# Performance work log

Measured on AMD Instinct MI355X. Metric: run time of the kernel, lower is better.

Reference implementation:

```python
import jax, jax.numpy as jnp
import numpy as np

LAMBDA_WEIGHT = 1.0


def _soft_argmax(logits):
    # differentiable_argmax: sum_c softmax(logits)[c] * c along class dim
    nc = logits.shape[1]
    probs = jax.nn.softmax(logits, axis=1)
    idx = jnp.arange(nc, dtype=logits.dtype)[None, :, None, None]
    return jnp.sum(probs * idx, axis=1)  # [B, H, W]


def _pair_loss(mask, d):
    # mask: [L] bool over row-major flattened HxW; d: [L] float (col - row).
    # torch.where returns row-major order, coord[:,1]-coord[:,0] == d at masked
    # pixels; second diff is |d_i - d_prev| over consecutive masked pixels.
    L = mask.shape[0]
    pos = jnp.where(mask, jnp.arange(L), -1)
    last = jax.lax.cummax(pos, axis=0)                 # last masked index <= i
    prev = jnp.concatenate([jnp.full((1,), -1), last[:-1]])  # strictly before i
    valid = mask & (prev >= 0)
    dprev = d[jnp.clip(prev, 0, L - 1)]
    s = jnp.sum(jnp.where(valid, jnp.abs(d - dprev), 0.0))
    npairs = jnp.sum(valid)
    npts = jnp.sum(mask)
    mean = s / jnp.maximum(npairs, 1).astype(d.dtype)
    # N==0 contributes 0 (the `continue`); N==1 gives an empty-mean (NaN) in
    # torch -- guarded to 0 here (such degenerate classes are skipped).
    return jnp.where(npts >= 2, mean / (npts + 1).astype(d.dtype), 0.0)


def reference(logits, labels):
    bs, nc, h, w = logits.shape
    seg = jnp.floor(jax.lax.stop_gradient(_soft_argmax(logits))).astype(jnp.int32)
    seg = seg.reshape(bs, h * w)                       # [B, L] row-major
    # d[i] = col - row for flattened index i
    i = jnp.arange(h * w)
    d = ((i % w) - (i // w)).astype(jnp.float32)       # [L]
    classes = jnp.arange(1, nc, dtype=jnp.int32)       # skip background c=0
    masks = seg[:, None, :] == classes[None, :, None]  # [B, nc-1, L]
    per = jax.vmap(jax.vmap(_pair_loss, in_axes=(0, None)), in_axes=(0, None))(masks, d)
    return jnp.sum(per) * LAMBDA_WEIGHT


def setup_inputs() -> dict:
    key = jax.random.key(0)
    k1, k2 = jax.random.split(key)
    logits = jax.random.normal(k1, (16, 7, 368, 640), dtype=jnp.float32)
    labels = jax.random.randint(k2, (16, 368, 640), 0, 7, dtype=jnp.int64)
    return {"logits": logits, "labels": labels}
```

## Files before the change

### kernel.cpp

```cpp
#include <hip/hip_runtime.h>
#include <cstdint>
#include <cstddef>

#define BB 16
#define CC 7
#define HH 368
#define WW 640
#define LL (HH * WW)
#define NCLS 6
#define NCOMBO (BB * NCLS)
#define PXW 256
#define PXB 1024
#define BPB (LL / PXB)
#define NBLK (BB * BPB)

struct St { int S, cnt, first, last; };

__device__ inline St comb(const St& a, const St& b) {
    St r;
    int both = (a.cnt > 0) & (b.cnt > 0);
    r.S     = a.S + b.S + (both ? abs(b.first - a.last) : 0);
    r.cnt   = a.cnt + b.cnt;
    r.first = (a.cnt > 0) ? a.first : b.first;
    r.last  = (b.cnt > 0) ? b.last : a.last;
    return r;
}

__device__ inline St shfl_down_st(const St& s, int off) {
    St r;
    r.S     = __shfl_down(s.S, off, 64);
    r.cnt   = __shfl_down(s.cnt, off, 64);
    r.first = __shfl_down(s.first, off, 64);
    r.last  = __shfl_down(s.last, off, 64);
    return r;
}

__global__ __launch_bounds__(256) void fused_kernel(const float* __restrict__ logits,
                                                    int4* __restrict__ blkStates) {
    int blk = blockIdx.x;
    int b   = blk / BPB;
    int bb  = blk - b * BPB;
    int t   = threadIdx.x;
    int w   = t >> 6;
    int lane = t & 63;
    int i   = bb * PXB + w * PXW + lane * 4;
    const float* base = logits + (size_t)b * CC * LL + i;

    float x[CC][4];
#pragma unroll
    for (int c = 0; c < CC; ++c) {
        float4 v = *reinterpret_cast<const float4*>(base + (size_t)c * LL);
        x[c][0] = v.x; x[c][1] = v.y; x[c][2] = v.z; x[c][3] = v.w;
    }

    int row = i / WW;
    int col = i - row * WW;
    int d0  = col - row;

    St st[NCLS];
#pragma unroll
    for (int c = 0; c < NCLS; ++c) { st[c].S = 0; st[c].cnt = 0; st[c].first = 0; st[c].last = 0; }

#pragma unroll
    for (int k = 0; k < 4; ++k) {
        float m = x[0][k];
#pragma unroll
        for (int c = 1; c < CC; ++c) m = fmaxf(m, x[c][k]);
        float s = 0.0f, wsum = 0.0f;
#pragma unroll
        for (int c = 0; c < CC; ++c) {
            float e = __expf(x[c][k] - m);
            s += e;
            wsum += e * (float)c;
        }
        int sv = (int)floorf(__fdividef(wsum, s));
        int d  = d0 + k;
#pragma unroll
        for (int c = 0; c < NCLS; ++c) {
            if (sv == c + 1) {
                if (st[c].cnt == 0) st[c].first = d;
                else                st[c].S += abs(d - st[c].last);
                st[c].last = d;
                st[c].cnt++;
            }
        }
    }

    __shared__ int4 sw[NCLS][4];

#pragma unroll
    for (int c = 0; c < NCLS; ++c) {
        St s = st[c];
        if (__ballot(s.cnt > 0) == 0ull) {
            if (lane == 0) sw[c][w] = make_int4(0, 0, 0, 0);
            continue;
        }
#pragma unroll
        for (int off = 1; off < 64; off <<= 1) {
            St o = shfl_down_st(s, off);
            s = comb(s, o);
        }
        if (lane == 0) sw[c][w] = make_int4(s.S, s.cnt, s.first, s.last);
    }
    __syncthreads();

    if (t < NCLS) {
        St acc{sw[t][0].x, sw[t][0].y, sw[t][0].z, sw[t][0].w};
#pragma unroll
        for (int q = 1; q < 4; ++q) {
            St o{sw[t][q].x, sw[t][q].y, sw[t][q].z, sw[t][q].w};
            acc = comb(acc, o);
        }
        blkStates[(size_t)t * NBLK + blk] = make_int4(acc.S, acc.cnt, acc.first, acc.last);
    }
}

__global__ __launch_bounds__(256) void combine_kernel(const int4* __restrict__ blkStates,
                                                      float* __restrict__ out) {
    int combo = blockIdx.x;
    int b = combo / NCLS;
    int c = combo - b * NCLS;
    int t = threadIdx.x;

    St st{0, 0, 0, 0};
    if (t < BPB) {
        int4 v = blkStates[(size_t)c * NBLK + b * BPB + t];
        st = St{v.x, v.y, v.z, v.w};
    }

#pragma unroll
    for (int off = 1; off < 64; off <<= 1) {
        St o = shfl_down_st(st, off);
        st = comb(st, o);
    }

    __shared__ int4 ws[4];
    int wave = t >> 6;
    if ((t & 63) == 0) ws[wave] = make_int4(st.S, st.cnt, st.first, st.last);
    __syncthreads();

    if (t == 0) {
        St acc{ws[0].x, ws[0].y, ws[0].z, ws[0].w};
#pragma unroll
        for (int w = 1; w < 4; ++w) {
            St o{ws[w].x, ws[w].y, ws[w].z, ws[w].w};
            acc = comb(acc, o);
        }
        int n = acc.cnt;
        if (n >= 2) {
            double res = ((double)acc.S / (double)(n - 1)) / (double)(n + 1);
            atomicAdd(out, (float)res);
        }
    }
}

extern "C" void kernel_launch(void* const* d_in, const int* in_sizes, int n_in,
                              void* d_out, int out_size, void* d_ws, size_t ws_size,
                              hipStream_t stream) {
    const float* logits = (const float*)d_in[0];
    float* out = (float*)d_out;

    int4* blkStates = (int4*)d_ws;

    hipMemsetAsync(out, 0, sizeof(float) * out_size, stream);
    fused_kernel<<<NBLK, 256, 0, stream>>>(logits, blkStates);
    combine_kernel<<<NCOMBO, 256, 0, stream>>>(blkStates, out);
}
```

Before: 166.7 us.

## Process larger tiles per block with shared-memory seg staging and sequential per-thread scan

Each block now handles 5120 pixels: it first computes soft-argmax labels coalesced into packed bytes in shared memory, then each thread scans 20 consecutive pixels serially before the wave and block reductions. This cuts the block count and the number of per-class shuffle reductions per pixel, and it lets the combine kernel use a single wave with no shared-memory stage. In exchange it adds a shared-memory round trip and a barrier. The per-thread serial loop over 20 pixels and 6 classes may also raise register use and branch divergence.

```diff
diff --git a/kernel.cpp b/kernel.cpp
--- a/kernel.cpp
+++ b/kernel.cpp
@@ -9,10 +9,10 @@
 #define LL (HH * WW)
 #define NCLS 6
 #define NCOMBO (BB * NCLS)
-#define PXW 256
-#define PXB 1024
-#define BPB (LL / PXB)
+#define TILE 5120
+#define BPB (LL / TILE)
 #define NBLK (BB * BPB)
+#define PPT (TILE / 256)
 
 struct St { int S, cnt, first, last; };
 
@@ -43,37 +43,58 @@
     int t   = threadIdx.x;
     int w   = t >> 6;
     int lane = t & 63;
-    int i   = bb * PXB + w * PXW + lane * 4;
-    const float* base = logits + (size_t)b * CC * LL + i;
 
-    float x[CC][4];
+    __shared__ uint32_t segw[TILE / 4];
+    __shared__ int4 sw[NCLS][4];
+
+    const float* lbase = logits + (size_t)b * CC * LL;
+
 #pragma unroll
-    for (int c = 0; c < CC; ++c) {
-        float4 v = *reinterpret_cast<const float4*>(base + (size_t)c * LL);
-        x[c][0] = v.x; x[c][1] = v.y; x[c][2] = v.z; x[c][3] = v.w;
+    for (int j = 0; j < TILE / 1024; ++j) {
+        int px = bb * TILE + j * 1024 + t * 4;
+        const float* base = lbase + px;
+        float x[CC][4];
+#pragma unroll
+        for (int c = 0; c < CC; ++c) {
+            float4 v = *reinterpret_cast<const float4*>(base + (size_t)c * LL);
+            x[c][0] = v.x; x[c][1] = v.y; x[c][2] = v.z; x[c][3] = v.w;
+        }
+        uint32_t packed = 0;
+#pragma unroll
+        for (int k = 0; k < 4; ++k) {
+            float m = x[0][k];
+#pragma unroll
+            for (int c = 1; c < CC; ++c) m = fmaxf(m, x[c][k]);
+            float s = 0.0f, wsum = 0.0f;
+#pragma unroll
+            for (int c = 0; c < CC; ++c) {
+                float e = __expf(x[c][k] - m);
+                s += e;
+                wsum += e * (float)c;
+            }
+            int sv = (int)floorf(__fdividef(wsum, s));
+            packed |= (uint32_t)sv << (8 * k);
+        }
+        segw[j * 256 + t] = packed;
     }
+    __syncthreads();
 
-    int row = i / WW;
-    int col = i - row * WW;
+    int gpx = bb * TILE + t * PPT;
+    int row = gpx / WW;
+    int col = gpx - row * WW;
     int d0  = col - row;
+
+    uint32_t wbuf[PPT / 4];
+#pragma unroll
+    for (int j = 0; j < PPT / 4; ++j) wbuf[j] = segw[t * (PPT / 4) + j];
 
     St st[NCLS];
 #pragma unroll
     for (int c = 0; c < NCLS; ++c) { st[c].S = 0; st[c].cnt = 0; st[c].first = 0; st[c].last = 0; }
 
 #pragma unroll
-    for (int k = 0; k < 4; ++k) {
-        float m = x[0][k];
-#pragma unroll
-        for (int c = 1; c < CC; ++c) m = fmaxf(m, x[c][k]);
-        float s = 0.0f, wsum = 0.0f;
-#pragma unroll
-        for (int c = 0; c < CC; ++c) {
-            float e = __expf(x[c][k] - m);
-            s += e;
-            wsum += e * (float)c;
-        }
-        int sv = (int)floorf(__fdividef(wsum, s));
+    for (int k = 0; k < PPT; ++k) {
+        int sv = (int)((wbuf[k >> 2] >> (8 * (k & 3))) & 0xFFu);
         int d  = d0 + k;
 #pragma unroll
         for (int c = 0; c < NCLS; ++c) {
@@ -86,15 +107,9 @@
         }
     }
 
-    __shared__ int4 sw[NCLS][4];
-
 #pragma unroll
     for (int c = 0; c < NCLS; ++c) {
         St s = st[c];
-        if (__ballot(s.cnt > 0) == 0ull) {
-            if (lane == 0) sw[c][w] = make_int4(0, 0, 0, 0);
-            continue;
-        }
 #pragma unroll
         for (int off = 1; off < 64; off <<= 1) {
             St o = shfl_down_st(s, off);
@@ -115,8 +130,8 @@
     }
 }
 
-__global__ __launch_bounds__(256) void combine_kernel(const int4* __restrict__ blkStates,
-                                                      float* __restrict__ out) {
+__global__ __launch_bounds__(64) void combine_kernel(const int4* __restrict__ blkStates,
+                                                     float* __restrict__ out) {
     int combo = blockIdx.x;
     int b = combo / NCLS;
     int c = combo - b * NCLS;
@@ -134,21 +149,10 @@
         st = comb(st, o);
     }
 
-    __shared__ int4 ws[4];
-    int wave = t >> 6;
-    if ((t & 63) == 0) ws[wave] = make_int4(st.S, st.cnt, st.first, st.last);
-    __syncthreads();
-
     if (t == 0) {
-        St acc{ws[0].x, ws[0].y, ws[0].z, ws[0].w};
-#pragma unroll
-        for (int w = 1; w < 4; ++w) {
-            St o{ws[w].x, ws[w].y, ws[w].z, ws[w].w};
-            acc = comb(acc, o);
-        }
-        int n = acc.cnt;
+        int n = st.cnt;
         if (n >= 2) {
-            double res = ((double)acc.S / (double)(n - 1)) / (double)(n + 1);
+            double res = ((double)st.S / (double)(n - 1)) / (double)(n + 1);
             atomicAdd(out, (float)res);
         }
     }
@@ -164,5 +168,5 @@
 
     hipMemsetAsync(out, 0, sizeof(float) * out_size, stream);
     fused_kernel<<<NBLK, 256, 0, stream>>>(logits, blkStates);
-    combine_kernel<<<NCOMBO, 256, 0, stream>>>(blkStates, out);
+    combine_kernel<<<NCOMBO, 64, 0, stream>>>(blkStates, out);
 }
```

Result: slower. 173.8 us (+4.2%).
